# Kernel optimization log

Hardware: AMD Instinct MI355X
Metric: run time of the kernel (lower is better)

## Reference

```python
import jax, jax.numpy as jnp
import numpy as np

B, C, H, W = 8, 3, 1024, 1024
N_SPOTS = int(H * W * 0.015)  # 15728, matches torch: n = int(H*W*0.015)
KSIZE, SIGMA = 5, 1.5
RMAX = 3  # max snow-box radius (torch.randint(1, 4))


def setup_inputs() -> dict:
    key = jax.random.key(0)
    k1, k2, k3, k4 = jax.random.split(key, 4)
    x = jax.random.uniform(k1, (B, C, H, W), dtype=jnp.float32)
    ys = jax.random.randint(k2, (B, N_SPOTS), 0, H)
    xs = jax.random.randint(k3, (B, N_SPOTS), 0, W)
    rs = jax.random.randint(k4, (B, N_SPOTS), 0, 3)  # radius = rs + 1 in {1,2,3}
    return {"x": x, "ys": ys, "xs": xs, "rs": rs}


def _snow_mask(ys, xs, rs, h, w):
    # Union of axis-aligned boxes: pixel (py,px) is snow iff some spot has
    # |py - y| <= r and |px - x| <= r (box clipping to the image is equivalent).
    b, n = ys.shape
    r = rs + 1  # radii 1..3
    d = jnp.arange(-RMAX, RMAX + 1)
    dy = jnp.repeat(d, 2 * RMAX + 1)  # [49]
    dx = jnp.tile(d, 2 * RMAX + 1)    # [49]
    yy = ys[:, :, None] + dy  # [B, n, 49]
    xx = xs[:, :, None] + dx
    valid = ((jnp.abs(dy) <= r[:, :, None]) & (jnp.abs(dx) <= r[:, :, None])
             & (yy >= 0) & (yy < h) & (xx >= 0) & (xx < w))
    yy = jnp.where(valid, yy, h)  # out-of-bounds sentinel -> dropped by scatter
    xx = jnp.where(valid, xx, w)
    b_idx = jnp.broadcast_to(jnp.arange(b)[:, None, None], yy.shape)
    mask = jnp.zeros((b, h, w), dtype=bool)
    mask = mask.at[b_idx, yy, xx].set(True, mode="drop")
    return mask


def _gauss_kernel():
    coords = jnp.arange(KSIZE, dtype=jnp.float32) - KSIZE // 2
    g = jnp.exp(-coords ** 2 / (2.0 * SIGMA ** 2))
    g = g / g.sum()
    return jnp.outer(g, g)  # [5, 5]


def reference(x, ys, xs, rs):
    b, c, h, w = x.shape
    mask = _snow_mask(ys, xs, rs, h, w)                   # [B, H, W]
    out = jnp.where(mask[:, None, :, :], jnp.float32(0.95), x)
    kernel = jnp.broadcast_to(_gauss_kernel(), (c, 1, KSIZE, KSIZE))  # depthwise OIHW
    pad = KSIZE // 2
    out = jax.lax.conv_general_dilated(
        out, kernel, window_strides=(1, 1), padding=[(pad, pad), (pad, pad)],
        dimension_numbers=("NCHW", "OIHW", "NCHW"), feature_group_count=c)
    return jnp.clip(out, 0.0, 1.0)
```

## Files before the change

### kernel.cpp

```cpp
#include <hip/hip_runtime.h>

#define BB 8
#define CC 3
#define HH 1024
#define WW 1024
#define NS 15728
#define NG (NS / 4)

#define G0 0.1200784f
#define G1 0.2338808f
#define G2 0.2920816f

#define NSTRIPE 32

__global__ __launch_bounds__(256) void snow_mask_kernel(
    const int* __restrict__ ys, const int* __restrict__ xs,
    const int* __restrict__ rs, unsigned int* __restrict__ mbits) {
  __shared__ unsigned int lm[HH];
  const int b = blockIdx.y;
  const int sx0 = blockIdx.x << 5;
  const int tid = threadIdx.x;

  for (int i = tid; i < HH; i += 256) lm[i] = 0u;
  __syncthreads();

  const int4* __restrict__ y4 = (const int4*)(ys + b * NS);
  const int4* __restrict__ x4 = (const int4*)(xs + b * NS);
  const int4* __restrict__ r4 = (const int4*)(rs + b * NS);

  auto spot = [&](int y, int x, int r) {
    r += 1;
    int x0 = max(x - r, sx0), x1 = min(x + r, sx0 + 31);
    if (x0 > x1) return;
    int y0 = max(y - r, 0), y1 = min(y + r, HH - 1);
    unsigned m = (0xFFFFFFFFu << (x0 & 31)) & (0xFFFFFFFFu >> (31 - (x1 & 31)));
    for (int py = y0; py <= y1; ++py) atomicOr(&lm[py], m);
  };

  int g = tid;
  int4 Y = {0, 0, 0, 0}, X = {0, 0, 0, 0}, R = {0, 0, 0, 0};
  bool have = g < NG;
  if (have) { Y = y4[g]; X = x4[g]; R = r4[g]; }
  while (have) {
    int gn = g + 256;
    int4 Yn = {0, 0, 0, 0}, Xn = {0, 0, 0, 0}, Rn = {0, 0, 0, 0};
    bool haven = gn < NG;
    if (haven) { Yn = y4[gn]; Xn = x4[gn]; Rn = r4[gn]; }
    spot(Y.x, X.x, R.x);
    spot(Y.y, X.y, R.y);
    spot(Y.z, X.z, R.z);
    spot(Y.w, X.w, R.w);
    g = gn; Y = Yn; X = Xn; R = Rn; have = haven;
  }
  __syncthreads();

  unsigned int* dst = mbits + ((unsigned)(b * HH) << 5) + blockIdx.x;
  for (int i = tid; i < HH; i += 256) dst[i << 5] = lm[i];
}

#define RROWS 16

struct Row {
  float4 B;
  float2 L;
  float2 R;
  unsigned m0, m1;
};

__global__ __launch_bounds__(256, 4) void snow_blur_kernel(
    const float* __restrict__ x, const unsigned int* __restrict__ mbits,
    float* __restrict__ out) {
  const int bz = blockIdx.y;
  const int b = bz / CC;
  const int gy0 = blockIdx.x * RROWS;
  const int tid = threadIdx.x;
  const int col = tid << 2;

  const float* __restrict__ xp = x + (size_t)bz * (HH * WW);
  const unsigned int* __restrict__ mb = mbits + ((unsigned)(b * HH) << 5);

  const int cL = max(col - 2, 0);
  const int cR = min(col + 4, WW - 2);
  const unsigned loob = (col == 0) ? 16u : 0u;
  const unsigned roob = (col == WW - 4) ? 16u : 0u;
  const int w = cL >> 5;
  const int w2 = min(w + 1, 31);
  const int bpL = cL - (w << 5);
  const int bpB = col - (w << 5);
  const int bpR = col + 4 - (w << 5);

  auto loadrow = [&](int gy, Row& rw) {
    int gyc = min(max(gy, 0), HH - 1);
    const float* rp = xp + ((size_t)gyc << 10);
    const unsigned* mrow = mb + (gyc << 5);
    rw.B = *(const float4*)(rp + col);
    rw.L = *(const float2*)(rp + cL);
    rw.R = *(const float2*)(rp + cR);
    rw.m0 = mrow[w];
    rw.m1 = mrow[w2];
  };

  auto consume = [&](const Row& rw, unsigned ro) {
    unsigned long long mw =
        (unsigned long long)rw.m0 | ((unsigned long long)rw.m1 << 32);
    unsigned bL = ((unsigned)(mw >> bpL) & 3u) | ro | loob;
    unsigned bB = ((unsigned)(mw >> bpB) & 0xFu) | ro;
    unsigned bR = ((unsigned)(mw >> bpR) & 3u) | ro | roob;
    float2 fL;
    fL.x = (bL & 1u) ? 0.95f : rw.L.x;
    fL.y = (bL & 2u) ? 0.95f : rw.L.y;
    if (bL & 16u) { fL.x = 0.f; fL.y = 0.f; }
    float4 fB;
    fB.x = (bB & 1u) ? 0.95f : rw.B.x;
    fB.y = (bB & 2u) ? 0.95f : rw.B.y;
    fB.z = (bB & 4u) ? 0.95f : rw.B.z;
    fB.w = (bB & 8u) ? 0.95f : rw.B.w;
    if (bB & 16u) { fB.x = 0.f; fB.y = 0.f; fB.z = 0.f; fB.w = 0.f; }
    float2 fR;
    fR.x = (bR & 1u) ? 0.95f : rw.R.x;
    fR.y = (bR & 2u) ? 0.95f : rw.R.y;
    if (bR & 16u) { fR.x = 0.f; fR.y = 0.f; }
    float4 h;
    h.x = G0 * (fL.x + fB.z) + G1 * (fL.y + fB.y) + G2 * fB.x;
    h.y = G0 * (fL.y + fB.w) + G1 * (fB.x + fB.z) + G2 * fB.y;
    h.z = G0 * (fB.x + fR.x) + G1 * (fB.y + fB.w) + G2 * fB.z;
    h.w = G0 * (fB.y + fR.y) + G1 * (fB.z + fR.x) + G2 * fB.w;
    return h;
  };

  auto rof = [&](int gy) { return (gy < 0 || gy >= HH) ? 16u : 0u; };

  Row p0, p1, p2, p3, s0, s1, s2;
  loadrow(gy0 - 2, p0);
  loadrow(gy0 - 1, p1);
  loadrow(gy0 + 0, p2);
  loadrow(gy0 + 1, p3);
  loadrow(gy0 + 2, s0);
  loadrow(gy0 + 3, s1);
  loadrow(gy0 + 4, s2);
  float4 h0 = consume(p0, rof(gy0 - 2));
  float4 h1 = consume(p1, rof(gy0 - 1));
  float4 h2 = consume(p2, 0u);
  float4 h3 = consume(p3, 0u);

  float* op = out + (size_t)bz * (HH * WW) + ((size_t)gy0 << 10) + col;
#pragma unroll
  for (int k = 0; k < RROWS; ++k) {
    Row nr{};
    if (k < RROWS - 3) loadrow(gy0 + 5 + k, nr);

    float4 h4 = consume(s0, rof(gy0 + 2 + k));

    float4 s;
    s.x = G0 * (h0.x + h4.x) + G1 * (h1.x + h3.x) + G2 * h2.x;
    s.y = G0 * (h0.y + h4.y) + G1 * (h1.y + h3.y) + G2 * h2.y;
    s.z = G0 * (h0.z + h4.z) + G1 * (h1.z + h3.z) + G2 * h2.z;
    s.w = G0 * (h0.w + h4.w) + G1 * (h1.w + h3.w) + G2 * h2.w;
    s.x = fminf(fmaxf(s.x, 0.f), 1.f);
    s.y = fminf(fmaxf(s.y, 0.f), 1.f);
    s.z = fminf(fmaxf(s.z, 0.f), 1.f);
    s.w = fminf(fmaxf(s.w, 0.f), 1.f);
    *(float4*)op = s;
    op += WW;

    s0 = s1; s1 = s2; s2 = nr;
    h0 = h1; h1 = h2; h2 = h3; h3 = h4;
  }
}

extern "C" void kernel_launch(void* const* d_in, const int* in_sizes, int n_in,
                              void* d_out, int out_size, void* d_ws, size_t ws_size,
                              hipStream_t stream) {
  const float* x = (const float*)d_in[0];
  const int* ys = (const int*)d_in[1];
  const int* xs = (const int*)d_in[2];
  const int* rs = (const int*)d_in[3];
  float* out = (float*)d_out;

  unsigned int* mbits = (unsigned int*)d_ws;

  dim3 mgrid(NSTRIPE, BB);
  snow_mask_kernel<<<mgrid, 256, 0, stream>>>(ys, xs, rs, mbits);

  dim3 grid(HH / RROWS, BB * CC);
  snow_blur_kernel<<<grid, 256, 0, stream>>>(x, mbits, out);
}
```

Baseline: 205.4 us.

## Stage blur tiles into LDS via direct global-to-LDS loads with shuffle-based halo

Measured after the change: 203.6 us. About the same (-0.9%).

```diff
diff --git a/kernel.cpp b/kernel.cpp
--- a/kernel.cpp
+++ b/kernel.cpp
@@ -58,68 +58,108 @@
   for (int i = tid; i < HH; i += 256) dst[i << 5] = lm[i];
 }
 
-#define RROWS 16
-
-struct Row {
-  float4 B;
-  float2 L;
-  float2 R;
-  unsigned m0, m1;
-};
+#define TCOLS 256
+#define TROWS 32
+#define SROWS 36
+
+__device__ __forceinline__ void gl_lds16(const float* g, float* l) {
+  __builtin_amdgcn_global_load_lds(
+      (const __attribute__((address_space(1))) void*)g,
+      (__attribute__((address_space(3))) void*)l, 16, 0, 0);
+}
+__device__ __forceinline__ void gl_lds4(const void* g, void* l) {
+  __builtin_amdgcn_global_load_lds(
+      (const __attribute__((address_space(1))) void*)g,
+      (__attribute__((address_space(3))) void*)l, 4, 0, 0);
+}
 
 __global__ __launch_bounds__(256, 4) void snow_blur_kernel(
     const float* __restrict__ x, const unsigned int* __restrict__ mbits,
     float* __restrict__ out) {
-  const int bz = blockIdx.y;
+  __shared__ float s_img[SROWS * TCOLS];
+  __shared__ float s_halo[192];
+  __shared__ unsigned s_msk[SROWS * 16];
+
+  const int bz = blockIdx.z;
   const int b = bz / CC;
-  const int gy0 = blockIdx.x * RROWS;
+  const int gy0 = blockIdx.y * TROWS;
+  const int col0 = blockIdx.x * TCOLS;
   const int tid = threadIdx.x;
-  const int col = tid << 2;
+  const int wv = tid >> 6;
+  const int lane = tid & 63;
 
   const float* __restrict__ xp = x + (size_t)bz * (HH * WW);
   const unsigned int* __restrict__ mb = mbits + ((unsigned)(b * HH) << 5);
-
-  const int cL = max(col - 2, 0);
-  const int cR = min(col + 4, WW - 2);
-  const unsigned loob = (col == 0) ? 16u : 0u;
-  const unsigned roob = (col == WW - 4) ? 16u : 0u;
-  const int w = cL >> 5;
-  const int w2 = min(w + 1, 31);
-  const int bpL = cL - (w << 5);
-  const int bpB = col - (w << 5);
-  const int bpR = col + 4 - (w << 5);
-
-  auto loadrow = [&](int gy, Row& rw) {
-    int gyc = min(max(gy, 0), HH - 1);
-    const float* rp = xp + ((size_t)gyc << 10);
-    const unsigned* mrow = mb + (gyc << 5);
-    rw.B = *(const float4*)(rp + col);
-    rw.L = *(const float2*)(rp + cL);
-    rw.R = *(const float2*)(rp + cR);
-    rw.m0 = mrow[w];
-    rw.m1 = mrow[w2];
-  };
-
-  auto consume = [&](const Row& rw, unsigned ro) {
-    unsigned long long mw =
-        (unsigned long long)rw.m0 | ((unsigned long long)rw.m1 << 32);
-    unsigned bL = ((unsigned)(mw >> bpL) & 3u) | ro | loob;
-    unsigned bB = ((unsigned)(mw >> bpB) & 0xFu) | ro;
-    unsigned bR = ((unsigned)(mw >> bpR) & 3u) | ro | roob;
-    float2 fL;
-    fL.x = (bL & 1u) ? 0.95f : rw.L.x;
-    fL.y = (bL & 2u) ? 0.95f : rw.L.y;
-    if (bL & 16u) { fL.x = 0.f; fL.y = 0.f; }
+  const int w0b = col0 >> 5;
+
+#pragma unroll
+  for (int i = 0; i < 9; ++i) {
+    int s = wv + (i << 2);
+    int gy = min(max(gy0 - 2 + s, 0), HH - 1);
+    gl_lds16(xp + ((size_t)gy << 10) + col0 + (lane << 2), &s_img[s * TCOLS]);
+  }
+  if (wv == 0) {
+#pragma unroll
+    for (int i = 0; i < 3; ++i) {
+      int e = (i << 6) + lane;
+      int s = min(e >> 2, SROWS - 1);
+      int j = e & 3;
+      int gy = min(max(gy0 - 2 + s, 0), HH - 1);
+      int cc = (j < 2) ? (col0 - 2 + j) : (col0 + 254 + j);
+      cc = min(max(cc, 0), WW - 1);
+      gl_lds4(xp + ((size_t)gy << 10) + cc, &s_halo[i << 6]);
+    }
+  } else {
+#pragma unroll
+    for (int i = 0; i < 3; ++i) {
+      int n = (wv - 1) * 3 + i;
+      int e = (n << 6) + lane;
+      int s = e >> 4;
+      int j = e & 15;
+      int gy = min(max(gy0 - 2 + s, 0), HH - 1);
+      int widx = min(max(w0b - 1 + j, 0), 31);
+      gl_lds4(mb + (gy << 5) + widx, &s_msk[n << 6]);
+    }
+  }
+  __syncthreads();
+
+  const bool l0 = (lane == 0), l63 = (lane == 63);
+  const int col = col0 + (lane << 2);
+  const unsigned eoob = (l0 && col0 == 0) ? 16u
+                        : ((l63 && col == WW - 4) ? 16u : 0u);
+  const int s5 = (lane & 7) << 2;
+  const int mj = 1 + (lane >> 3);
+  const int ej = l63 ? 9 : 0;
+  const int eshift = l63 ? 0 : 30;
+  const int ehw = l63 ? 2 : 0;
+
+  auto hrow = [&](int s) {
+    int gr = gy0 - 2 + s;
+    unsigned ro = (gr < 0 || gr >= HH) ? 16u : 0u;
+    float4 B = *(const float4*)&s_img[s * TCOLS + (lane << 2)];
+    unsigned mw = s_msk[(s << 4) + mj];
+    unsigned bB = ((mw >> s5) & 0xFu) | ro;
     float4 fB;
-    fB.x = (bB & 1u) ? 0.95f : rw.B.x;
-    fB.y = (bB & 2u) ? 0.95f : rw.B.y;
-    fB.z = (bB & 4u) ? 0.95f : rw.B.z;
-    fB.w = (bB & 8u) ? 0.95f : rw.B.w;
+    fB.x = (bB & 1u) ? 0.95f : B.x;
+    fB.y = (bB & 2u) ? 0.95f : B.y;
+    fB.z = (bB & 4u) ? 0.95f : B.z;
+    fB.w = (bB & 8u) ? 0.95f : B.w;
     if (bB & 16u) { fB.x = 0.f; fB.y = 0.f; fB.z = 0.f; fB.w = 0.f; }
-    float2 fR;
-    fR.x = (bR & 1u) ? 0.95f : rw.R.x;
-    fR.y = (bR & 2u) ? 0.95f : rw.R.y;
-    if (bR & 16u) { fR.x = 0.f; fR.y = 0.f; }
+    unsigned emw = s_msk[(s << 4) + ej];
+    unsigned bE = ((emw >> eshift) & 3u) | ro | eoob;
+    float2 fE = *(const float2*)&s_halo[(s << 2) + ehw];
+    fE.x = (bE & 1u) ? 0.95f : fE.x;
+    fE.y = (bE & 2u) ? 0.95f : fE.y;
+    if (bE & 16u) { fE.x = 0.f; fE.y = 0.f; }
+    float lz = __shfl_up(fB.z, 1, 64);
+    float lw = __shfl_up(fB.w, 1, 64);
+    float rx = __shfl_down(fB.x, 1, 64);
+    float ry = __shfl_down(fB.y, 1, 64);
+    float2 fL, fR;
+    fL.x = l0 ? fE.x : lz;
+    fL.y = l0 ? fE.y : lw;
+    fR.x = l63 ? fE.x : rx;
+    fR.y = l63 ? fE.y : ry;
     float4 h;
     h.x = G0 * (fL.x + fB.z) + G1 * (fL.y + fB.y) + G2 * fB.x;
     h.y = G0 * (fL.y + fB.w) + G1 * (fB.x + fB.z) + G2 * fB.y;
@@ -128,42 +168,28 @@
     return h;
   };
 
-  auto rof = [&](int gy) { return (gy < 0 || gy >= HH) ? 16u : 0u; };
-
-  Row p0, p1, p2, p3, s0, s1, s2;
-  loadrow(gy0 - 2, p0);
-  loadrow(gy0 - 1, p1);
-  loadrow(gy0 + 0, p2);
-  loadrow(gy0 + 1, p3);
-  loadrow(gy0 + 2, s0);
-  loadrow(gy0 + 3, s1);
-  loadrow(gy0 + 4, s2);
-  float4 h0 = consume(p0, rof(gy0 - 2));
-  float4 h1 = consume(p1, rof(gy0 - 1));
-  float4 h2 = consume(p2, 0u);
-  float4 h3 = consume(p3, 0u);
-
-  float* op = out + (size_t)bz * (HH * WW) + ((size_t)gy0 << 10) + col;
-#pragma unroll
-  for (int k = 0; k < RROWS; ++k) {
-    Row nr{};
-    if (k < RROWS - 3) loadrow(gy0 + 5 + k, nr);
-
-    float4 h4 = consume(s0, rof(gy0 + 2 + k));
-
-    float4 s;
-    s.x = G0 * (h0.x + h4.x) + G1 * (h1.x + h3.x) + G2 * h2.x;
-    s.y = G0 * (h0.y + h4.y) + G1 * (h1.y + h3.y) + G2 * h2.y;
-    s.z = G0 * (h0.z + h4.z) + G1 * (h1.z + h3.z) + G2 * h2.z;
-    s.w = G0 * (h0.w + h4.w) + G1 * (h1.w + h3.w) + G2 * h2.w;
-    s.x = fminf(fmaxf(s.x, 0.f), 1.f);
-    s.y = fminf(fmaxf(s.y, 0.f), 1.f);
-    s.z = fminf(fmaxf(s.z, 0.f), 1.f);
-    s.w = fminf(fmaxf(s.w, 0.f), 1.f);
-    *(float4*)op = s;
+  const int sbase = wv << 3;
+  float4 h0 = hrow(sbase + 0);
+  float4 h1 = hrow(sbase + 1);
+  float4 h2 = hrow(sbase + 2);
+  float4 h3 = hrow(sbase + 3);
+
+  float* op = out + (size_t)bz * (HH * WW) +
+              ((size_t)(gy0 + (wv << 3)) << 10) + col;
+#pragma unroll
+  for (int k = 0; k < 8; ++k) {
+    float4 h4 = hrow(sbase + 4 + k);
+    float4 sv;
+    sv.x = G0 * (h0.x + h4.x) + G1 * (h1.x + h3.x) + G2 * h2.x;
+    sv.y = G0 * (h0.y + h4.y) + G1 * (h1.y + h3.y) + G2 * h2.y;
+    sv.z = G0 * (h0.z + h4.z) + G1 * (h1.z + h3.z) + G2 * h2.z;
+    sv.w = G0 * (h0.w + h4.w) + G1 * (h1.w + h3.w) + G2 * h2.w;
+    sv.x = fminf(fmaxf(sv.x, 0.f), 1.f);
+    sv.y = fminf(fmaxf(sv.y, 0.f), 1.f);
+    sv.z = fminf(fmaxf(sv.z, 0.f), 1.f);
+    sv.w = fminf(fmaxf(sv.w, 0.f), 1.f);
+    *(float4*)op = sv;
     op += WW;
-
-    s0 = s1; s1 = s2; s2 = nr;
     h0 = h1; h1 = h2; h2 = h3; h3 = h4;
   }
 }
@@ -182,6 +208,6 @@
   dim3 mgrid(NSTRIPE, BB);
   snow_mask_kernel<<<mgrid, 256, 0, stream>>>(ys, xs, rs, mbits);
 
-  dim3 grid(HH / RROWS, BB * CC);
+  dim3 grid(WW / TCOLS, HH / TROWS, BB * CC);
   snow_blur_kernel<<<grid, 256, 0, stream>>>(x, mbits, out);
 }
```
